# Kernel tuning notes

Hardware: AMD Instinct MI355X
Metric: run time of the kernel (lower is better)

## Reference

```python
import jax, jax.numpy as jnp
import numpy as np

DIM = 256
HEADS = 8
HD = DIM // HEADS  # 32
WS = 8             # window size
N = WS * WS        # 64 tokens per window
BN_SCALE = 1.0 / np.sqrt(1.0 + 1e-5)  # BatchNorm with default running stats (mean 0, var 1)


def _relative_position_index():
    # static int index table [N, N], computed with numpy (matches torch buffer)
    coords = np.stack(np.meshgrid(np.arange(WS), np.arange(WS), indexing='ij'))  # (2, ws, ws)
    cf = coords.reshape(2, -1)                                                   # (2, N)
    rel = cf[:, :, None] - cf[:, None, :]                                        # (2, N, N)
    rel = rel.transpose(1, 2, 0)                                                 # (N, N, 2)
    rel[:, :, 0] += WS - 1
    rel[:, :, 1] += WS - 1
    rel[:, :, 0] *= 2 * WS - 1
    return jnp.asarray(rel.sum(-1))  # (N, N)


def _relative_coords_table():
    # static float table [(2ws-1), (2ws-1), 2] with Swin-V2 log-spaced coords
    r = np.arange(-(WS - 1), WS, dtype=np.float32)
    g = np.stack(np.meshgrid(r, r, indexing='ij'), axis=-1)  # (L, L, 2)
    g = g / (WS - 1) * 8.0
    g = np.sign(g) * np.log2(np.abs(g) + 1.0) / np.log2(8.0)
    return jnp.asarray(g)


def setup_inputs() -> dict:
    key = jax.random.key(0)
    ks = jax.random.split(key, 9)
    B, H, W = 16, 64, 64
    s = 0.02
    return {
        'x': jax.random.normal(ks[0], (B, DIM, H, W), dtype=jnp.float32),
        'qkv_w': jax.random.normal(ks[1], (3 * DIM, DIM), dtype=jnp.float32) * s,
        'qkv_b': jax.random.normal(ks[2], (3 * DIM,), dtype=jnp.float32) * s,
        'proj_w': jax.random.normal(ks[3], (DIM, DIM), dtype=jnp.float32) * s,
        'proj_b': jax.random.normal(ks[4], (DIM,), dtype=jnp.float32) * s,
        'cpb_w1': jax.random.normal(ks[5], (DIM, 2), dtype=jnp.float32) * 0.5,
        'cpb_b1': jax.random.normal(ks[6], (DIM,), dtype=jnp.float32) * 0.5,
        'cpb_w2': jax.random.normal(ks[7], (HEADS, DIM), dtype=jnp.float32) * 0.1,
        'dw_w': jax.random.normal(ks[8], (DIM, 1, 7, 7), dtype=jnp.float32) * s,
    }


def reference(x, qkv_w, qkv_b, proj_w, proj_b, cpb_w1, cpb_b1, cpb_w2, dw_w):
    B, C, H, W = x.shape
    Hn, Wn = H // WS, W // WS
    B_ = B * Hn * Wn

    # continuous position bias: pointwise MLP (conv1x1+BN+SiLU, conv1x1+BN)
    tbl = _relative_coords_table()                          # (L, L, 2)
    h = jax.nn.silu((tbl @ cpb_w1.T + cpb_b1) * BN_SCALE)   # (L, L, DIM)
    bias_table = (h @ cpb_w2.T) * BN_SCALE                  # (L, L, HEADS)
    bias_table = bias_table.reshape(-1, HEADS)
    rpi = _relative_position_index()
    bias = bias_table[rpi.reshape(-1)].reshape(N, N, HEADS).transpose(2, 0, 1)
    bias = 16.0 * jax.nn.sigmoid(bias)                      # (HEADS, N, N)

    # qkv 1x1 conv, window partition
    qkv = jnp.einsum('oc,bchw->bohw', qkv_w, x) + qkv_b[None, :, None, None]
    win = qkv.reshape(B, 3 * C, Hn, WS, Wn, WS).transpose(0, 2, 4, 1, 3, 5)
    win = win.reshape(B_, 3 * C, N)
    qkvw = win.reshape(B_, 3, HEADS, HD, N).transpose(1, 0, 2, 4, 3)  # (3, B_, H, N, hd)
    q, k, v = qkvw[0], qkvw[1], qkvw[2]

    # SDPA with additive bias (attn_mask)
    scores = jnp.einsum('bhnd,bhmd->bhnm', q, k) / np.sqrt(HD) + bias[None]
    attn = jax.nn.softmax(scores, axis=-1)
    o = jnp.einsum('bhnm,bhmd->bhnd', attn, v)

    def window_reverse(w):  # (B_, N, C) -> (B, C, H, W)
        t = w.reshape(B, Hn, Wn, WS, WS, C).transpose(0, 5, 1, 3, 2, 4)
        return t.reshape(B, C, H, W)

    x_img = window_reverse(o.transpose(0, 2, 1, 3).reshape(B_, N, C))
    v_img = window_reverse(v.transpose(0, 2, 1, 3).reshape(B_, N, C))

    # depthwise 7x7 positional encoding on v, residual add
    pe = jax.lax.conv_general_dilated(
        v_img, dw_w, window_strides=(1, 1), padding='SAME',
        feature_group_count=C, dimension_numbers=('NCHW', 'OIHW', 'NCHW'))
    out = x_img + pe
    out = jnp.einsum('oc,bchw->bohw', proj_w, out) + proj_b[None, :, None, None]
    return out
```

## Files before the change

kernel.cpp:

```cpp
#include <hip/hip_runtime.h>
#include <cstdint>
#include <cstddef>

typedef unsigned short u16;
typedef unsigned int   u32;

#define LW     15
#define BNS    0.9999950000374997f
#define SCALE  0.17677669529663687f

typedef __bf16 bf16x8 __attribute__((ext_vector_type(8)));
typedef float  f32x4  __attribute__((ext_vector_type(4)));

__device__ __forceinline__ u16 f2bf(float f){
  union { float f; u32 i; } v; v.f = f;
  u32 r = v.i + 0x7FFFu + ((v.i >> 16) & 1u);
  return (u16)(r >> 16);
}
__device__ __forceinline__ float bf2f(u16 u){
  union { u32 i; float f; } v; v.i = ((u32)u) << 16; return v.f;
}

__global__ void k_cvt_w(const float* __restrict__ qw, const float* __restrict__ pw,
                        u16* __restrict__ qwb, u16* __restrict__ pwb){
  const int i = blockIdx.x*256 + threadIdx.x;
  if (i < 196608) qwb[i] = f2bf(qw[i]);
  else            pwb[i - 196608] = f2bf(pw[i - 196608]);
}

__global__ void k_cpb_mlp(const float* __restrict__ w1, const float* __restrict__ b1,
                          const float* __restrict__ w2, float* __restrict__ tab){
  const int e = blockIdx.x;
  const int c = threadIdx.x;
  const float a0 = (float)(e / LW - 7);
  const float a1 = (float)(e % LW - 7);
  const float cx = copysignf(log2f(fabsf(a0)*(8.f/7.f) + 1.f) * (1.f/3.f), a0);
  const float cy = copysignf(log2f(fabsf(a1)*(8.f/7.f) + 1.f) * (1.f/3.f), a1);
  float pre = (cx*w1[2*c] + cy*w1[2*c+1] + b1[c]) * BNS;
  float hid = pre / (1.f + __expf(-pre));
  __shared__ float hl[256];
  hl[c] = hid;
  __syncthreads();
  if (c < 8){
    float s = 0.f;
    for (int i = 0; i < 256; ++i) s += hl[i] * w2[c*256 + i];
    tab[e*8 + c] = s * BNS;
  }
}

__global__ void k_bias_expand(const float* __restrict__ tab, float* __restrict__ biasT){
  const int id = blockIdx.x*256 + threadIdx.x;
  const int nq = id & 63;
  const int m  = (id >> 6) & 63;
  const int h  = id >> 12;
  const int dy = (nq >> 3) - (m >> 3) + 7;
  const int dx = (nq & 7)  - (m & 7)  + 7;
  const float v = tab[(dy*LW + dx)*8 + h];
  biasT[id] = 16.f / (1.f + __expf(-v));
}

__global__ __launch_bounds__(256, 2) void k_qkv_attn(
    const float* __restrict__ x, const u16* __restrict__ qwb,
    const float* __restrict__ qb, const float* __restrict__ biasT,
    float* __restrict__ xout, u16* __restrict__ vout){
  const int win = blockIdx.x;
  const int b = win >> 6, wy = (win >> 3) & 7, wx = win & 7;
  __shared__ __align__(16) char smem[80384];
  u16*   xs   = (u16*)(smem);
  u16*   q_b  = (u16*)(smem + 33792);
  u16*   ks_  = (u16*)(smem + 52224);
  u16*   vsT  = (u16*)(smem + 70656);
  float* linv = (float*)(smem + 79872);

  const float* xbase = x + (size_t)b*256*4096 + (size_t)(wy*8)*64 + wx*8;
  for (int i = threadIdx.x; i < 16384; i += 256){
    const int c = i >> 6, n = i & 63;
    xs[n*264 + c] = f2bf(xbase[(size_t)c*4096 + ((n>>3)<<6) + (n&7)]);
  }
  const int wave = threadIdx.x >> 6, lane = threadIdx.x & 63;
  const int quad = lane >> 4, l16 = lane & 15;

  const int ed = threadIdx.x >> 3;
  const int eq = (threadIdx.x & 7) * 8;
  const size_t epix = (size_t)(wy*8 + (threadIdx.x & 7))*64 + wx*8;

  const f32x4 zero4 = {0.f, 0.f, 0.f, 0.f};
  const int qn = wave*16 + l16;

  __syncthreads();

  for (int p = 0; p < 4; ++p){
    #pragma unroll
    for (int j = 0; j < 3; ++j){
      const int rt  = wave*3 + j;
      const int sec = rt >> 2;
      const int hs  = (rt >> 1) & 1;
      const int dl  = (rt & 1) * 16;
      const int oga = sec*256 + (p*2 + hs)*32 + dl + l16;
      bf16x8 af[8];
      #pragma unroll
      for (int kc = 0; kc < 8; ++kc)
        af[kc] = *(const bf16x8*)(qwb + (size_t)oga*256 + kc*32 + quad*8);
      const float4 bias4 = *(const float4*)&qb[sec*256 + (p*2 + hs)*32 + dl + quad*4];
      const int ddo = hs*32 + dl + quad*4;
      #pragma unroll
      for (int tt = 0; tt < 4; ++tt){
        f32x4 acc = zero4;
        #pragma unroll
        for (int kc = 0; kc < 8; ++kc){
          bf16x8 bf = *(const bf16x8*)&xs[(tt*16 + l16)*264 + kc*32 + quad*8];
          acc = __builtin_amdgcn_mfma_f32_16x16x32_bf16(af[kc], bf, acc, 0, 0, 0);
        }
        const int tok = tt*16 + l16;
        if (sec < 2){
          ushort4 pk;
          pk.x = f2bf(acc[0] + bias4.x);
          pk.y = f2bf(acc[1] + bias4.y);
          pk.z = f2bf(acc[2] + bias4.z);
          pk.w = f2bf(acc[3] + bias4.w);
          u16* dst = (sec == 0) ? q_b : ks_;
          *(ushort4*)&dst[tok*72 + ddo] = pk;
        } else {
          #pragma unroll
          for (int r = 0; r < 4; ++r)
            vsT[(ddo + r)*72 + tok] = f2bf(acc[r] + ((const float*)&bias4)[r]);
        }
      }
    }
    __syncthreads();

    bf16x8 qf2[2];
    qf2[0] = *(const bf16x8*)&q_b[qn*72 +  0 + quad*8];
    qf2[1] = *(const bf16x8*)&q_b[qn*72 + 32 + quad*8];
    #pragma unroll
    for (int h2 = 0; h2 < 2; ++h2){
      const int h = p*2 + h2;
      f32x4 st[4];
      #pragma unroll
      for (int kt = 0; kt < 4; ++kt){
        bf16x8 ka = *(const bf16x8*)&ks_[(kt*16 + l16)*72 + h2*32 + quad*8];
        st[kt] = __builtin_amdgcn_mfma_f32_16x16x32_bf16(ka, qf2[h2], zero4, 0, 0, 0);
      }
      float sc[16], mx = -1e30f;
      #pragma unroll
      for (int kt = 0; kt < 4; ++kt)
        #pragma unroll
        for (int r = 0; r < 4; ++r){
          const int key = kt*16 + quad*4 + r;
          const float v = st[kt][r]*SCALE + biasT[(h<<12) + (key<<6) + qn];
          sc[kt*4+r] = v; mx = fmaxf(mx, v);
        }
      mx = fmaxf(mx, __shfl_xor(mx, 16));
      mx = fmaxf(mx, __shfl_xor(mx, 32));
      float sum = 0.f;
      #pragma unroll
      for (int i = 0; i < 16; ++i){ sc[i] = __expf(sc[i] - mx); sum += sc[i]; }
      sum += __shfl_xor(sum, 16);
      sum += __shfl_xor(sum, 32);
      if (quad == 0) linv[h2*64 + qn] = 1.f / sum;
      u16* P = (u16*)(smem + 33792 + h2*9216);
      #pragma unroll
      for (int kt = 0; kt < 4; ++kt){
        ushort4 pk;
        pk.x = f2bf(sc[kt*4+0]); pk.y = f2bf(sc[kt*4+1]);
        pk.z = f2bf(sc[kt*4+2]); pk.w = f2bf(sc[kt*4+3]);
        *(ushort4*)&P[qn*72 + kt*16 + quad*4] = pk;
      }
    }
    __syncthreads();

    #pragma unroll
    for (int h2 = 0; h2 < 2; ++h2){
      const u16* P = (const u16*)(smem + 33792 + h2*9216);
      float* obuf  = (float*)(smem + 52224 + h2*9216);
      bf16x8 pa0 = *(const bf16x8*)&P[qn*72 +  0 + quad*8];
      bf16x8 pa1 = *(const bf16x8*)&P[qn*72 + 32 + quad*8];
      #pragma unroll
      for (int dt = 0; dt < 2; ++dt){
        bf16x8 bv0 = *(const bf16x8*)&vsT[(h2*32 + dt*16 + l16)*72 +  0 + quad*8];
        bf16x8 bv1 = *(const bf16x8*)&vsT[(h2*32 + dt*16 + l16)*72 + 32 + quad*8];
        f32x4 o = __builtin_amdgcn_mfma_f32_16x16x32_bf16(pa0, bv0, zero4, 0, 0, 0);
        o = __builtin_amdgcn_mfma_f32_16x16x32_bf16(pa1, bv1, o, 0, 0, 0);
        #pragma unroll
        for (int r = 0; r < 4; ++r){
          const float ls = linv[h2*64 + wave*16 + quad*4 + r];
          obuf[(dt*16 + l16)*72 + wave*16 + quad*4 + r] = o[r]*ls;
        }
      }
    }
    __syncthreads();

    #pragma unroll
    for (int h2 = 0; h2 < 2; ++h2){
      const float* obuf = (const float*)(smem + 52224 + h2*9216);
      const size_t gp = ((size_t)(b*256 + (p*2 + h2)*32 + ed))*4096 + epix;
      float4 o0 = *(const float4*)&obuf[ed*72 + eq];
      float4 o1 = *(const float4*)&obuf[ed*72 + eq + 4];
      *(float4*)&xout[gp]     = o0;
      *(float4*)&xout[gp + 4] = o1;
      ushort4 v0 = *(const ushort4*)&vsT[(h2*32 + ed)*72 + eq];
      ushort4 v1 = *(const ushort4*)&vsT[(h2*32 + ed)*72 + eq + 4];
      *(ushort4*)&vout[gp]     = v0;
      *(ushort4*)&vout[gp + 4] = v1;
    }
    __syncthreads();
  }
}

__global__ __launch_bounds__(256) void k_dwconv(
    const u16* __restrict__ vimg, const float* __restrict__ dww,
    float* __restrict__ io){
  const int b = blockIdx.x >> 8, c = blockIdx.x & 255;
  __shared__ float tile[70*72];
  const size_t base = ((size_t)(b*256 + c)) * 4096;
  for (int i = threadIdx.x; i < 70*72; i += 256) tile[i] = 0.f;
  float w[49];
  #pragma unroll
  for (int j = 0; j < 49; ++j) w[j] = dww[c*49 + j];
  __syncthreads();
  for (int i = threadIdx.x; i < 4096; i += 256){
    const int y = i >> 6, xx = i & 63;
    tile[(y+3)*72 + (xx+3)] = bf2f(vimg[base + i]);
  }
  __syncthreads();

  const int x0 = (threadIdx.x & 15) * 4;
  const int y0 = (threadIdx.x >> 4) * 4;
  float acc[4][4];
  #pragma unroll
  for (int i = 0; i < 4; ++i)
    #pragma unroll
    for (int j = 0; j < 4; ++j) acc[i][j] = 0.f;

  #pragma unroll
  for (int ty = 0; ty < 10; ++ty){
    const float* rp = &tile[(y0 + ty)*72 + x0];
    float r[12];
    *(float4*)&r[0] = *(const float4*)&rp[0];
    *(float4*)&r[4] = *(const float4*)&rp[4];
    *(float4*)&r[8] = *(const float4*)&rp[8];
    #pragma unroll
    for (int oy = 0; oy < 4; ++oy){
      if (ty >= oy && ty - oy <= 6){
        const int ky = ty - oy;
        #pragma unroll
        for (int ox = 0; ox < 4; ++ox)
          #pragma unroll
          for (int kx = 0; kx < 7; ++kx)
            acc[oy][ox] += w[ky*7 + kx] * r[ox + kx];
      }
    }
  }
  #pragma unroll
  for (int oy = 0; oy < 4; ++oy){
    const size_t gi = base + (size_t)(y0 + oy)*64 + x0;
    float4 res = *(const float4*)&io[gi];
    res.x += acc[oy][0]; res.y += acc[oy][1];
    res.z += acc[oy][2]; res.w += acc[oy][3];
    *(float4*)&io[gi] = res;
  }
}

__global__ void k_proj(const u16* __restrict__ pwb, const float* __restrict__ pb,
                       float* __restrict__ io){
  const int row = blockIdx.x;
  const int b = row >> 6, y = row & 63;
  __shared__ __align__(16) u16 ts[64*264];
  const float* tbase = io + (size_t)b*256*4096 + (size_t)y*64;
  for (int i = threadIdx.x; i < 16384; i += 256){
    const int c = i >> 6, n = i & 63;
    ts[n*264 + c] = f2bf(tbase[(size_t)c*4096 + n]);
  }
  __syncthreads();
  const int wave = threadIdx.x >> 6, lane = threadIdx.x & 63;
  const int quad = lane >> 4, l16 = lane & 15;
  for (int oi = 0; oi < 4; ++oi){
    const int ot = wave*4 + oi;
    const int orow = ot*16 + l16;
    bf16x8 af[8];
    #pragma unroll
    for (int kc = 0; kc < 8; ++kc)
      af[kc] = *reinterpret_cast<const bf16x8*>(pwb + (size_t)orow*256 + kc*32 + quad*8);
    #pragma unroll
    for (int nt = 0; nt < 4; ++nt){
      f32x4 acc = {0.f, 0.f, 0.f, 0.f};
      #pragma unroll
      for (int kc = 0; kc < 8; ++kc){
        bf16x8 bf = *reinterpret_cast<const bf16x8*>(&ts[(nt*16 + l16)*264 + kc*32 + quad*8]);
        acc = __builtin_amdgcn_mfma_f32_16x16x32_bf16(af[kc], bf, acc, 0, 0, 0);
      }
      #pragma unroll
      for (int r = 0; r < 4; ++r){
        const int o = ot*16 + quad*4 + r;
        io[((size_t)(b*256 + o))*4096 + (size_t)y*64 + nt*16 + l16] = acc[r] + pb[o];
      }
    }
  }
}

extern "C" void kernel_launch(void* const* d_in, const int* in_sizes, int n_in,
                              void* d_out, int out_size, void* d_ws, size_t ws_size,
                              hipStream_t stream){
  const float* x   = (const float*)d_in[0];
  const float* qw  = (const float*)d_in[1];
  const float* qb  = (const float*)d_in[2];
  const float* pw  = (const float*)d_in[3];
  const float* pb  = (const float*)d_in[4];
  const float* w1  = (const float*)d_in[5];
  const float* b1  = (const float*)d_in[6];
  const float* w2  = (const float*)d_in[7];
  const float* dww = (const float*)d_in[8];

  char* ws = (char*)d_ws;
  float* tab   = (float*)(ws);
  float* biasT = (float*)(ws + 8192);
  u16*   qwb   = (u16*)  (ws + 139264);
  u16*   pwb   = (u16*)  (ws + 532480);
  u16*   vimg  = (u16*)  (ws + 663552);
  float* out   = (float*)d_out;

  k_cvt_w      <<<1024, 256, 0, stream>>>(qw, pw, qwb, pwb);
  k_cpb_mlp    <<<225,  256, 0, stream>>>(w1, b1, w2, tab);
  k_bias_expand<<<128,  256, 0, stream>>>(tab, biasT);
  k_qkv_attn   <<<1024, 256, 0, stream>>>(x, qwb, qb, biasT, out, vimg);
  k_dwconv     <<<4096, 256, 0, stream>>>(vimg, dww, out);
  k_proj       <<<1024, 256, 0, stream>>>(pwb, pb, out);
}
```

Before: 352.0 us.

## Vectorize global loads and restructure MFMA loops in qkv, dwconv and proj kernels

The input staging in the qkv/attention and projection kernels now reads float4 vectors instead of scalar floats. The dwconv kernel loads bf16 in 8-wide vectors and zeroes its tile with float4 stores, and the v output store is merged into one 16-byte write. The qkv GEMM now keeps all three weight row-tiles in registers and reuses each shared-memory B fragment across them, and the projection GEMM reuses B fragments across two output tiles. This trades higher register pressure for fewer memory instructions and more MFMA issue density.

```diff
diff --git a/kernel.cpp b/kernel.cpp
--- a/kernel.cpp
+++ b/kernel.cpp
@@ -11,6 +11,7 @@
 
 typedef __bf16 bf16x8 __attribute__((ext_vector_type(8)));
 typedef float  f32x4  __attribute__((ext_vector_type(4)));
+typedef u16    u16x8  __attribute__((ext_vector_type(8)));
 
 __device__ __forceinline__ u16 f2bf(float f){
   union { float f; u32 i; } v; v.f = f;
@@ -73,9 +74,16 @@
   float* linv = (float*)(smem + 79872);
 
   const float* xbase = x + (size_t)b*256*4096 + (size_t)(wy*8)*64 + wx*8;
-  for (int i = threadIdx.x; i < 16384; i += 256){
-    const int c = i >> 6, n = i & 63;
-    xs[n*264 + c] = f2bf(xbase[(size_t)c*4096 + ((n>>3)<<6) + (n&7)]);
+  for (int i = threadIdx.x; i < 4096; i += 256){
+    const int c  = i >> 4;
+    const int g  = i & 15;
+    const int py = g >> 1, xh = (g & 1) * 4;
+    float4 v4 = *(const float4*)&xbase[(size_t)c*4096 + py*64 + xh];
+    const int n0 = py*8 + xh;
+    xs[(n0+0)*264 + c] = f2bf(v4.x);
+    xs[(n0+1)*264 + c] = f2bf(v4.y);
+    xs[(n0+2)*264 + c] = f2bf(v4.z);
+    xs[(n0+3)*264 + c] = f2bf(v4.w);
   }
   const int wave = threadIdx.x >> 6, lane = threadIdx.x & 63;
   const int quad = lane >> 4, l16 = lane & 15;
@@ -90,6 +98,8 @@
   __syncthreads();
 
   for (int p = 0; p < 4; ++p){
+    bf16x8 af[3][8];
+    float4 bias4[3];
     #pragma unroll
     for (int j = 0; j < 3; ++j){
       const int rt  = wave*3 + j;
@@ -97,33 +107,51 @@
       const int hs  = (rt >> 1) & 1;
       const int dl  = (rt & 1) * 16;
       const int oga = sec*256 + (p*2 + hs)*32 + dl + l16;
-      bf16x8 af[8];
       #pragma unroll
       for (int kc = 0; kc < 8; ++kc)
-        af[kc] = *(const bf16x8*)(qwb + (size_t)oga*256 + kc*32 + quad*8);
-      const float4 bias4 = *(const float4*)&qb[sec*256 + (p*2 + hs)*32 + dl + quad*4];
-      const int ddo = hs*32 + dl + quad*4;
-      #pragma unroll
-      for (int tt = 0; tt < 4; ++tt){
-        f32x4 acc = zero4;
-        #pragma unroll
-        for (int kc = 0; kc < 8; ++kc){
-          bf16x8 bf = *(const bf16x8*)&xs[(tt*16 + l16)*264 + kc*32 + quad*8];
-          acc = __builtin_amdgcn_mfma_f32_16x16x32_bf16(af[kc], bf, acc, 0, 0, 0);
-        }
-        const int tok = tt*16 + l16;
-        if (sec < 2){
-          ushort4 pk;
-          pk.x = f2bf(acc[0] + bias4.x);
-          pk.y = f2bf(acc[1] + bias4.y);
-          pk.z = f2bf(acc[2] + bias4.z);
-          pk.w = f2bf(acc[3] + bias4.w);
-          u16* dst = (sec == 0) ? q_b : ks_;
-          *(ushort4*)&dst[tok*72 + ddo] = pk;
-        } else {
-          #pragma unroll
-          for (int r = 0; r < 4; ++r)
-            vsT[(ddo + r)*72 + tok] = f2bf(acc[r] + ((const float*)&bias4)[r]);
+        af[j][kc] = *(const bf16x8*)(qwb + (size_t)oga*256 + kc*32 + quad*8);
+      bias4[j] = *(const float4*)&qb[sec*256 + (p*2 + hs)*32 + dl + quad*4];
+    }
+    #pragma unroll
+    for (int th = 0; th < 2; ++th){
+      f32x4 acc[3][2];
+      #pragma unroll
+      for (int j = 0; j < 3; ++j){ acc[j][0] = zero4; acc[j][1] = zero4; }
+      #pragma unroll
+      for (int kc = 0; kc < 8; ++kc){
+        bf16x8 b0 = *(const bf16x8*)&xs[((th*2+0)*16 + l16)*264 + kc*32 + quad*8];
+        bf16x8 b1 = *(const bf16x8*)&xs[((th*2+1)*16 + l16)*264 + kc*32 + quad*8];
+        #pragma unroll
+        for (int j = 0; j < 3; ++j){
+          acc[j][0] = __builtin_amdgcn_mfma_f32_16x16x32_bf16(af[j][kc], b0, acc[j][0], 0, 0, 0);
+          acc[j][1] = __builtin_amdgcn_mfma_f32_16x16x32_bf16(af[j][kc], b1, acc[j][1], 0, 0, 0);
+        }
+      }
+      #pragma unroll
+      for (int j = 0; j < 3; ++j){
+        const int rt  = wave*3 + j;
+        const int sec = rt >> 2;
+        const int hs  = (rt >> 1) & 1;
+        const int dl  = (rt & 1) * 16;
+        const int ddo = hs*32 + dl + quad*4;
+        #pragma unroll
+        for (int t2 = 0; t2 < 2; ++t2){
+          const int tok = (th*2 + t2)*16 + l16;
+          const f32x4 a = acc[j][t2];
+          if (sec < 2){
+            ushort4 pk;
+            pk.x = f2bf(a[0] + bias4[j].x);
+            pk.y = f2bf(a[1] + bias4[j].y);
+            pk.z = f2bf(a[2] + bias4[j].z);
+            pk.w = f2bf(a[3] + bias4[j].w);
+            u16* dst = (sec == 0) ? q_b : ks_;
+            *(ushort4*)&dst[tok*72 + ddo] = pk;
+          } else {
+            vsT[(ddo+0)*72 + tok] = f2bf(a[0] + bias4[j].x);
+            vsT[(ddo+1)*72 + tok] = f2bf(a[1] + bias4[j].y);
+            vsT[(ddo+2)*72 + tok] = f2bf(a[2] + bias4[j].z);
+            vsT[(ddo+3)*72 + tok] = f2bf(a[3] + bias4[j].w);
+          }
         }
       }
     }
@@ -198,10 +226,8 @@
       float4 o1 = *(const float4*)&obuf[ed*72 + eq + 4];
       *(float4*)&xout[gp]     = o0;
       *(float4*)&xout[gp + 4] = o1;
-      ushort4 v0 = *(const ushort4*)&vsT[(h2*32 + ed)*72 + eq];
-      ushort4 v1 = *(const ushort4*)&vsT[(h2*32 + ed)*72 + eq + 4];
-      *(ushort4*)&vout[gp]     = v0;
-      *(ushort4*)&vout[gp + 4] = v1;
+      u16x8 v8 = *(const u16x8*)&vsT[(h2*32 + ed)*72 + eq];
+      *(u16x8*)&vout[gp] = v8;
     }
     __syncthreads();
   }
@@ -213,14 +239,17 @@
   const int b = blockIdx.x >> 8, c = blockIdx.x & 255;
   __shared__ float tile[70*72];
   const size_t base = ((size_t)(b*256 + c)) * 4096;
-  for (int i = threadIdx.x; i < 70*72; i += 256) tile[i] = 0.f;
+  for (int i = threadIdx.x; i < 1260; i += 256)
+    *(float4*)&tile[i*4] = (float4){0.f, 0.f, 0.f, 0.f};
   float w[49];
   #pragma unroll
   for (int j = 0; j < 49; ++j) w[j] = dww[c*49 + j];
   __syncthreads();
-  for (int i = threadIdx.x; i < 4096; i += 256){
-    const int y = i >> 6, xx = i & 63;
-    tile[(y+3)*72 + (xx+3)] = bf2f(vimg[base + i]);
+  for (int i = threadIdx.x; i < 512; i += 256){
+    const int y = i >> 3, x8 = (i & 7) * 8;
+    u16x8 v = *(const u16x8*)&vimg[base + y*64 + x8];
+    #pragma unroll
+    for (int j = 0; j < 8; ++j) tile[(y+3)*72 + x8 + 3 + j] = bf2f(v[j]);
   }
   __syncthreads();
 
@@ -261,39 +290,62 @@
   }
 }
 
-__global__ void k_proj(const u16* __restrict__ pwb, const float* __restrict__ pb,
-                       float* __restrict__ io){
+__global__ __launch_bounds__(256) void k_proj(
+    const u16* __restrict__ pwb, const float* __restrict__ pb,
+    float* __restrict__ io){
   const int row = blockIdx.x;
   const int b = row >> 6, y = row & 63;
   __shared__ __align__(16) u16 ts[64*264];
   const float* tbase = io + (size_t)b*256*4096 + (size_t)y*64;
-  for (int i = threadIdx.x; i < 16384; i += 256){
-    const int c = i >> 6, n = i & 63;
-    ts[n*264 + c] = f2bf(tbase[(size_t)c*4096 + n]);
+  for (int i = threadIdx.x; i < 4096; i += 256){
+    const int c = i >> 4, n0 = (i & 15) * 4;
+    float4 v4 = *(const float4*)&tbase[(size_t)c*4096 + n0];
+    ts[(n0+0)*264 + c] = f2bf(v4.x);
+    ts[(n0+1)*264 + c] = f2bf(v4.y);
+    ts[(n0+2)*264 + c] = f2bf(v4.z);
+    ts[(n0+3)*264 + c] = f2bf(v4.w);
   }
   __syncthreads();
   const int wave = threadIdx.x >> 6, lane = threadIdx.x & 63;
   const int quad = lane >> 4, l16 = lane & 15;
-  for (int oi = 0; oi < 4; ++oi){
-    const int ot = wave*4 + oi;
-    const int orow = ot*16 + l16;
-    bf16x8 af[8];
-    #pragma unroll
-    for (int kc = 0; kc < 8; ++kc)
-      af[kc] = *reinterpret_cast<const bf16x8*>(pwb + (size_t)orow*256 + kc*32 + quad*8);
-    #pragma unroll
-    for (int nt = 0; nt < 4; ++nt){
-      f32x4 acc = {0.f, 0.f, 0.f, 0.f};
-      #pragma unroll
-      for (int kc = 0; kc < 8; ++kc){
-        bf16x8 bf = *reinterpret_cast<const bf16x8*>(&ts[(nt*16 + l16)*264 + kc*32 + quad*8]);
-        acc = __builtin_amdgcn_mfma_f32_16x16x32_bf16(af[kc], bf, acc, 0, 0, 0);
-      }
-      #pragma unroll
-      for (int r = 0; r < 4; ++r){
-        const int o = ot*16 + quad*4 + r;
-        io[((size_t)(b*256 + o))*4096 + (size_t)y*64 + nt*16 + l16] = acc[r] + pb[o];
-      }
+  const f32x4 zero4 = {0.f, 0.f, 0.f, 0.f};
+  #pragma unroll
+  for (int op = 0; op < 2; ++op){
+    bf16x8 af2[2][8];
+    #pragma unroll
+    for (int oj = 0; oj < 2; ++oj){
+      const int orow = (wave*4 + op*2 + oj)*16 + l16;
+      #pragma unroll
+      for (int kc = 0; kc < 8; ++kc)
+        af2[oj][kc] = *(const bf16x8*)(pwb + (size_t)orow*256 + kc*32 + quad*8);
+    }
+    f32x4 acc[2][4];
+    #pragma unroll
+    for (int oj = 0; oj < 2; ++oj)
+      #pragma unroll
+      for (int nt = 0; nt < 4; ++nt) acc[oj][nt] = zero4;
+    #pragma unroll
+    for (int kc = 0; kc < 8; ++kc){
+      bf16x8 bf[4];
+      #pragma unroll
+      for (int nt = 0; nt < 4; ++nt)
+        bf[nt] = *(const bf16x8*)&ts[(nt*16 + l16)*264 + kc*32 + quad*8];
+      #pragma unroll
+      for (int oj = 0; oj < 2; ++oj)
+        #pragma unroll
+        for (int nt = 0; nt < 4; ++nt)
+          acc[oj][nt] = __builtin_amdgcn_mfma_f32_16x16x32_bf16(af2[oj][kc], bf[nt], acc[oj][nt], 0, 0, 0);
+    }
+    #pragma unroll
+    for (int oj = 0; oj < 2; ++oj){
+      const int ot = wave*4 + op*2 + oj;
+      #pragma unroll
+      for (int nt = 0; nt < 4; ++nt)
+        #pragma unroll
+        for (int r = 0; r < 4; ++r){
+          const int o = ot*16 + quad*4 + r;
+          io[((size_t)(b*256 + o))*4096 + (size_t)y*64 + nt*16 + l16] = acc[oj][nt][r] + pb[o];
+        }
     }
   }
 }
```

Result: faster. 321.3 us (-8.7%).
